# Kernel optimization log

Hardware: AMD Instinct MI355X
Metric: run time of the kernel (lower is better)

Reference implementation:

```python
import jax, jax.numpy as jnp
import numpy as np

B, N, M, C = 64, 16384, 64, 512
OUT = 3 * M + 6  # 198
EPS = 1e-8


def setup_inputs() -> dict:
    key = jax.random.key(0)
    k0, k1, k2, k3 = jax.random.split(key, 4)
    x = jax.random.normal(k0, (B, C), jnp.float32)
    # previous write weighting: a valid distribution over N rows
    w_prev = jax.nn.softmax(jax.random.normal(k1, (B, N), jnp.float32), axis=-1)
    memory = jax.random.normal(k2, (B, N, M), jnp.float32) * 0.1
    W = jax.random.normal(k3, (C, OUT), jnp.float32) * (1.0 / np.sqrt(C))
    b = jnp.zeros((OUT,), jnp.float32)
    return {"x": x, "w_prev": w_prev, "memory": memory, "W": W, "b": b}


def _address(memory, k, beta, g, s, gamma, w_prev):
    # content addressing: cosine similarity between key k [B,M] and memory [B,N,M]
    dot = jnp.einsum('bnm,bm->bn', memory, k)
    denom = jnp.linalg.norm(memory, axis=-1) * jnp.linalg.norm(k, axis=-1, keepdims=True) + EPS
    w_c = jax.nn.softmax(beta * dot / denom, axis=-1)          # [B,N]
    # interpolation gate
    w_g = g * w_c + (1.0 - g) * w_prev                          # [B,N]
    # circular convolution over shifts [-1, 0, +1]
    w_s = (s[:, 0:1] * jnp.roll(w_g, -1, axis=-1)
           + s[:, 1:2] * w_g
           + s[:, 2:3] * jnp.roll(w_g, 1, axis=-1))             # [B,N]
    # sharpening
    w_sharp = jnp.power(w_s + EPS, gamma)                       # gamma [B,1]
    return w_sharp / jnp.sum(w_sharp, axis=-1, keepdims=True)


def reference(x, w_prev, memory, W, b):
    proj = x @ W + b                                            # [B, 3M+6]
    k = proj[:, :M]
    beta = jax.nn.softplus(proj[:, M:M + 1])
    g = jax.nn.sigmoid(proj[:, M + 1:M + 2])
    s = jax.nn.softmax(proj[:, M + 2:M + 5], axis=-1)
    gamma = 1.0 + jax.nn.softplus(proj[:, M + 5:M + 6])
    e = jax.nn.sigmoid(proj[:, M + 6:M + 6 + M])
    a = proj[:, M + 6 + M:]
    w = _address(memory, k, beta, g, s, gamma, w_prev)          # [B,N]
    # erase-add write: mem' = mem * (1 - w^T e) + w^T a
    erase = jnp.einsum('bn,bm->bnm', w, e)
    add = jnp.einsum('bn,bm->bnm', w, a)
    mem_new = memory * (1.0 - erase) + add
    return proj, w, mem_new
```

## Files before the change

### kernel.cpp

```cpp
#include <hip/hip_runtime.h>
#include <math.h>

#define BB   64
#define NN   16384
#define MM   64
#define CIN  512
#define OUTD 198
#define EPSF 1e-8f

#define NCHUNK (NN / 256)
#define NBLK   (BB * NCHUNK)

__device__ inline float softplusf(float v) {
    return v > 20.f ? v : log1pf(expf(v));
}
__device__ inline float sigmoidf(float v) {
    return 1.f / (1.f + expf(-v));
}

__global__ __launch_bounds__(256) void proj_kernel(
    const float* __restrict__ x, const float* __restrict__ W,
    const float* __restrict__ bias, float* __restrict__ out_proj,
    float* __restrict__ scal)
{
    const int b = blockIdx.x;
    const int tid = threadIdx.x;
    __shared__ __align__(16) float xs[CIN];
    __shared__ float pr[OUTD];

    for (int c = tid; c < CIN; c += 256) xs[c] = x[b * CIN + c];
    __syncthreads();

    if (tid < OUTD) {
        float acc = bias[tid];
        #pragma unroll 8
        for (int c = 0; c < CIN; ++c)
            acc = fmaf(xs[c], W[c * OUTD + tid], acc);
        out_proj[b * OUTD + tid] = acc;
        pr[tid] = acc;
    }
    __syncthreads();

    if (tid == 0) {
        float beta  = softplusf(pr[MM]);
        float g     = sigmoidf(pr[MM + 1]);
        float s0r = pr[MM + 2], s1r = pr[MM + 3], s2r = pr[MM + 4];
        float mx  = fmaxf(s0r, fmaxf(s1r, s2r));
        float e0 = expf(s0r - mx), e1 = expf(s1r - mx), e2 = expf(s2r - mx);
        float inv = 1.f / (e0 + e1 + e2);
        float gamma = 1.f + softplusf(pr[MM + 5]);
        float ksq = 0.f;
        for (int m = 0; m < MM; ++m) ksq += pr[m] * pr[m];
        float* sc = scal + b * 8;
        sc[0] = beta; sc[1] = g;
        sc[2] = e0 * inv; sc[3] = e1 * inv; sc[4] = e2 * inv;
        sc[5] = gamma; sc[6] = sqrtf(ksq);
    }
}

__global__ __launch_bounds__(256) void score_kernel(
    const float* __restrict__ mem, const float* __restrict__ proj,
    const float* __restrict__ scal, float* __restrict__ score,
    float* __restrict__ partials)
{
    const int b     = blockIdx.x >> 6;
    const int chunk = blockIdx.x & 63;
    const int tid   = threadIdx.x;
    const int n     = chunk * 256 + tid;

    __shared__ __align__(16) float ks[MM];
    __shared__ float red[8];

    if (tid < MM) ks[tid] = proj[b * OUTD + tid];
    __syncthreads();

    const float4* row = (const float4*)(mem + ((size_t)b * NN + n) * MM);
    float dot = 0.f, nsq = 0.f;
    #pragma unroll
    for (int i = 0; i < MM / 4; ++i) {
        float4 v  = row[i];
        float4 kv = *(const float4*)(&ks[i * 4]);
        dot += v.x * kv.x + v.y * kv.y + v.z * kv.z + v.w * kv.w;
        nsq += v.x * v.x + v.y * v.y + v.z * v.z + v.w * v.w;
    }
    const float beta  = scal[b * 8 + 0];
    const float knorm = scal[b * 8 + 6];
    const float sc = beta * dot / (sqrtf(nsq) * knorm + EPSF);
    score[(size_t)b * NN + n] = sc;

    float mv = sc;
    #pragma unroll
    for (int o = 32; o > 0; o >>= 1) mv = fmaxf(mv, __shfl_xor(mv, o));
    const int wid = tid >> 6, lane = tid & 63;
    if (lane == 0) red[wid] = mv;
    __syncthreads();
    if (tid == 0) red[4] = fmaxf(fmaxf(red[0], red[1]), fmaxf(red[2], red[3]));
    __syncthreads();
    const float mb = red[4];

    float ex = expf(sc - mb);
    #pragma unroll
    for (int o = 32; o > 0; o >>= 1) ex += __shfl_xor(ex, o);
    if (lane == 0) red[wid] = ex;
    __syncthreads();
    if (tid == 0) {
        partials[2 * blockIdx.x]     = mb;
        partials[2 * blockIdx.x + 1] = red[0] + red[1] + red[2] + red[3];
    }
}

__global__ __launch_bounds__(64) void combine_kernel(
    const float* __restrict__ partials, float* __restrict__ Mb,
    float* __restrict__ Sb, float* __restrict__ sumW)
{
    const int b = blockIdx.x, t = threadIdx.x;
    const float mb = partials[2 * (b * NCHUNK + t)];
    const float sb = partials[2 * (b * NCHUNK + t) + 1];
    float M = mb;
    #pragma unroll
    for (int o = 32; o > 0; o >>= 1) M = fmaxf(M, __shfl_xor(M, o));
    float contrib = sb * expf(mb - M);
    #pragma unroll
    for (int o = 32; o > 0; o >>= 1) contrib += __shfl_xor(contrib, o);
    if (t == 0) { Mb[b] = M; Sb[b] = contrib; sumW[b] = 0.f; }
}

__global__ __launch_bounds__(256) void sharp_kernel(
    const float* __restrict__ score, const float* __restrict__ w_prev,
    const float* __restrict__ scal, const float* __restrict__ Mb,
    const float* __restrict__ Sb, float* __restrict__ wsharp,
    float* __restrict__ sumW)
{
    const int b     = blockIdx.x >> 6;
    const int chunk = blockIdx.x & 63;
    const int tid   = threadIdx.x;
    const int start = chunk * 256;

    __shared__ float wg[258];
    __shared__ float red[8];

    const float g    = scal[b * 8 + 1];
    const float Mv   = Mb[b];
    const float invS = 1.f / Sb[b];
    const float* scb = score  + (size_t)b * NN;
    const float* wpb = w_prev + (size_t)b * NN;

    for (int i = tid; i < 258; i += 256) {
        const int idx = (start - 1 + i + NN) & (NN - 1);
        const float wc = expf(scb[idx] - Mv) * invS;
        wg[i] = g * wc + (1.f - g) * wpb[idx];
    }
    __syncthreads();

    const float s0 = scal[b * 8 + 2], s1 = scal[b * 8 + 3];
    const float s2 = scal[b * 8 + 4], gamma = scal[b * 8 + 5];
    const float ws  = s0 * wg[tid + 2] + s1 * wg[tid + 1] + s2 * wg[tid];
    const float wsh = powf(ws + EPSF, gamma);
    wsharp[(size_t)b * NN + start + tid] = wsh;

    float sum = wsh;
    #pragma unroll
    for (int o = 32; o > 0; o >>= 1) sum += __shfl_xor(sum, o);
    const int wid = tid >> 6, lane = tid & 63;
    if (lane == 0) red[wid] = sum;
    __syncthreads();
    if (tid == 0) atomicAdd(&sumW[b], red[0] + red[1] + red[2] + red[3]);
}

__global__ __launch_bounds__(256) void update_kernel(
    const float* __restrict__ mem, const float* __restrict__ proj,
    const float* __restrict__ wsharp, const float* __restrict__ sumW,
    float* __restrict__ out_w, float* __restrict__ out_mem)
{
    const int blk   = (int)gridDim.x - 1 - (int)blockIdx.x;
    const int b     = blk >> 6;
    const int chunk = blk & 63;
    const int tid   = threadIdx.x;
    const int n     = chunk * 256 + tid;

    __shared__ __align__(16) float es[MM];
    __shared__ __align__(16) float as_[MM];
    if (tid < MM) {
        es[tid]  = sigmoidf(proj[b * OUTD + MM + 6 + tid]);
        as_[tid] = proj[b * OUTD + MM + 6 + MM + tid];
    }
    __syncthreads();

    const float w = wsharp[(size_t)b * NN + n] / sumW[b];
    out_w[(size_t)b * NN + n] = w;

    const float4* row  = (const float4*)(mem     + ((size_t)b * NN + n) * MM);
    float4*       orow = (float4*)      (out_mem + ((size_t)b * NN + n) * MM);
    #pragma unroll
    for (int i = 0; i < MM / 4; ++i) {
        const float4 v  = row[i];
        const float4 e4 = *(const float4*)(&es[i * 4]);
        const float4 a4 = *(const float4*)(&as_[i * 4]);
        float4 r;
        r.x = v.x * (1.f - w * e4.x) + w * a4.x;
        r.y = v.y * (1.f - w * e4.y) + w * a4.y;
        r.z = v.z * (1.f - w * e4.z) + w * a4.z;
        r.w = v.w * (1.f - w * e4.w) + w * a4.w;
        orow[i] = r;
    }
}

extern "C" void kernel_launch(void* const* d_in, const int* in_sizes, int n_in,
                              void* d_out, int out_size, void* d_ws, size_t ws_size,
                              hipStream_t stream)
{
    const float* x      = (const float*)d_in[0];
    const float* w_prev = (const float*)d_in[1];
    const float* memory = (const float*)d_in[2];
    const float* W      = (const float*)d_in[3];
    const float* bias   = (const float*)d_in[4];

    float* out      = (float*)d_out;
    float* out_proj = out;
    float* out_w    = out + BB * OUTD;
    float* out_mem  = out_w + (size_t)BB * NN;

    float* ws_f     = (float*)d_ws;
    float* score    = ws_f;
    float* wsharp   = score + (size_t)BB * NN;
    float* partials = wsharp + (size_t)BB * NN;
    float* Mb       = partials + 2 * NBLK;
    float* Sb       = Mb + BB;
    float* sumW     = Sb + BB;
    float* scal     = sumW + BB;

    proj_kernel   <<<BB,   256, 0, stream>>>(x, W, bias, out_proj, scal);
    score_kernel  <<<NBLK, 256, 0, stream>>>(memory, out_proj, scal, score, partials);
    combine_kernel<<<BB,    64, 0, stream>>>(partials, Mb, Sb, sumW);
    sharp_kernel  <<<NBLK, 256, 0, stream>>>(score, w_prev, scal, Mb, Sb, wsharp, sumW);
    update_kernel <<<NBLK, 256, 0, stream>>>(memory, out_proj, wsharp, sumW, out_w, out_mem);
}
```

Baseline: 657.4 us.

## Coalesce memory reads in score and update kernels via row-split thread mapping

The score kernel now has 16 threads cooperate on each 64-float row, reading contiguous float4s and reducing the dot product and norm with shuffles, in place of one thread striding across a whole row. The update kernel is remapped so each thread handles consecutive float4s of the flat memory array, with 16384 blocks each covering 4096 floats. The erase sigmoid and add vectors are precomputed once per batch row in proj_kernel. The aim is fully coalesced global loads and stores on the two passes that stream the 256MB memory tensor, at the cost of extra shuffle reductions and redundant w loads.

```diff
diff --git a/kernel.cpp b/kernel.cpp
--- a/kernel.cpp
+++ b/kernel.cpp
@@ -10,6 +10,7 @@
 
 #define NCHUNK (NN / 256)
 #define NBLK   (BB * NCHUNK)
+#define UPD_BLKS 16384
 
 __device__ inline float softplusf(float v) {
     return v > 20.f ? v : log1pf(expf(v));
@@ -21,7 +22,7 @@
 __global__ __launch_bounds__(256) void proj_kernel(
     const float* __restrict__ x, const float* __restrict__ W,
     const float* __restrict__ bias, float* __restrict__ out_proj,
-    float* __restrict__ scal)
+    float* __restrict__ scal, float* __restrict__ ea)
 {
     const int b = blockIdx.x;
     const int tid = threadIdx.x;
@@ -41,6 +42,10 @@
     }
     __syncthreads();
 
+    if (tid < MM) {
+        ea[b * 128 + tid]      = sigmoidf(pr[MM + 6 + tid]);
+        ea[b * 128 + 64 + tid] = pr[MM + 6 + MM + tid];
+    }
     if (tid == 0) {
         float beta  = softplusf(pr[MM]);
         float g     = sigmoidf(pr[MM + 1]);
@@ -66,28 +71,41 @@
     const int b     = blockIdx.x >> 6;
     const int chunk = blockIdx.x & 63;
     const int tid   = threadIdx.x;
-    const int n     = chunk * 256 + tid;
+    const int rowbase = chunk * 256;
 
     __shared__ __align__(16) float ks[MM];
+    __shared__ float rowsc[256];
     __shared__ float red[8];
 
     if (tid < MM) ks[tid] = proj[b * OUTD + tid];
     __syncthreads();
 
-    const float4* row = (const float4*)(mem + ((size_t)b * NN + n) * MM);
-    float dot = 0.f, nsq = 0.f;
-    #pragma unroll
-    for (int i = 0; i < MM / 4; ++i) {
-        float4 v  = row[i];
-        float4 kv = *(const float4*)(&ks[i * 4]);
-        dot += v.x * kv.x + v.y * kv.y + v.z * kv.z + v.w * kv.w;
-        nsq += v.x * v.x + v.y * v.y + v.z * v.z + v.w * v.w;
-    }
     const float beta  = scal[b * 8 + 0];
     const float knorm = scal[b * 8 + 6];
-    const float sc = beta * dot / (sqrtf(nsq) * knorm + EPSF);
-    score[(size_t)b * NN + n] = sc;
-
+    const int sub = tid & 15;
+    const int rg  = tid >> 4;
+    const float4 kv = *(const float4*)(&ks[sub * 4]);
+    const float4* base = (const float4*)(mem + ((size_t)b * NN + rowbase) * MM);
+
+    #pragma unroll
+    for (int it = 0; it < 16; ++it) {
+        const float4 v = base[(it * 16 + rg) * 16 + sub];
+        float dot = v.x * kv.x + v.y * kv.y + v.z * kv.z + v.w * kv.w;
+        float nsq = v.x * v.x + v.y * v.y + v.z * v.z + v.w * v.w;
+        #pragma unroll
+        for (int o = 1; o < 16; o <<= 1) {
+            dot += __shfl_xor(dot, o);
+            nsq += __shfl_xor(nsq, o);
+        }
+        if (sub == 0) {
+            const float sc = beta * dot / (sqrtf(nsq) * knorm + EPSF);
+            score[(size_t)b * NN + rowbase + it * 16 + rg] = sc;
+            rowsc[it * 16 + rg] = sc;
+        }
+    }
+    __syncthreads();
+
+    const float sc = rowsc[tid];
     float mv = sc;
     #pragma unroll
     for (int o = 32; o > 0; o >>= 1) mv = fmaxf(mv, __shfl_xor(mv, o));
@@ -168,40 +186,40 @@
 }
 
 __global__ __launch_bounds__(256) void update_kernel(
-    const float* __restrict__ mem, const float* __restrict__ proj,
+    const float* __restrict__ mem, const float* __restrict__ ea_g,
     const float* __restrict__ wsharp, const float* __restrict__ sumW,
     float* __restrict__ out_w, float* __restrict__ out_mem)
 {
-    const int blk   = (int)gridDim.x - 1 - (int)blockIdx.x;
-    const int b     = blk >> 6;
-    const int chunk = blk & 63;
-    const int tid   = threadIdx.x;
-    const int n     = chunk * 256 + tid;
-
-    __shared__ __align__(16) float es[MM];
-    __shared__ __align__(16) float as_[MM];
-    if (tid < MM) {
-        es[tid]  = sigmoidf(proj[b * OUTD + MM + 6 + tid]);
-        as_[tid] = proj[b * OUTD + MM + 6 + MM + tid];
-    }
-    __syncthreads();
-
-    const float w = wsharp[(size_t)b * NN + n] / sumW[b];
-    out_w[(size_t)b * NN + n] = w;
-
-    const float4* row  = (const float4*)(mem     + ((size_t)b * NN + n) * MM);
-    float4*       orow = (float4*)      (out_mem + ((size_t)b * NN + n) * MM);
-    #pragma unroll
-    for (int i = 0; i < MM / 4; ++i) {
-        const float4 v  = row[i];
-        const float4 e4 = *(const float4*)(&es[i * 4]);
-        const float4 a4 = *(const float4*)(&as_[i * 4]);
+    const int blk = UPD_BLKS - 1 - (int)blockIdx.x;
+    const int tid = threadIdx.x;
+    const int b   = blk >> 8;
+
+    __shared__ __align__(16) float ea[128];
+    if (tid < 32) *(float4*)(&ea[tid * 4]) =
+        *(const float4*)(&ea_g[b * 128 + tid * 4]);
+    __syncthreads();
+
+    const int m = (tid * 4) & 63;
+    const float4 e4 = *(const float4*)(&ea[m]);
+    const float4 a4 = *(const float4*)(&ea[64 + m]);
+    const float invS = 1.0f / sumW[b];
+    const size_t base_f = (size_t)blk * 4096;
+    const float* wsb = wsharp + (size_t)b * NN;
+    float*       owb = out_w  + (size_t)b * NN;
+
+    #pragma unroll
+    for (int it = 0; it < 4; ++it) {
+        const size_t off = base_f + (size_t)it * 1024 + tid * 4;
+        const int n = (int)((off >> 6) & (NN - 1));
+        const float w = wsb[n] * invS;
+        if ((tid & 15) == 0) owb[n] = w;
+        const float4 v = *(const float4*)(mem + off);
         float4 r;
         r.x = v.x * (1.f - w * e4.x) + w * a4.x;
         r.y = v.y * (1.f - w * e4.y) + w * a4.y;
         r.z = v.z * (1.f - w * e4.z) + w * a4.z;
         r.w = v.w * (1.f - w * e4.w) + w * a4.w;
-        orow[i] = r;
+        *(float4*)(out_mem + off) = r;
     }
 }
 
@@ -228,10 +246,11 @@
     float* Sb       = Mb + BB;
     float* sumW     = Sb + BB;
     float* scal     = sumW + BB;
-
-    proj_kernel   <<<BB,   256, 0, stream>>>(x, W, bias, out_proj, scal);
-    score_kernel  <<<NBLK, 256, 0, stream>>>(memory, out_proj, scal, score, partials);
-    combine_kernel<<<BB,    64, 0, stream>>>(partials, Mb, Sb, sumW);
-    sharp_kernel  <<<NBLK, 256, 0, stream>>>(score, w_prev, scal, Mb, Sb, wsharp, sumW);
-    update_kernel <<<NBLK, 256, 0, stream>>>(memory, out_proj, wsharp, sumW, out_w, out_mem);
-}
+    float* ea       = scal + 8 * BB;
+
+    proj_kernel   <<<BB,      256, 0, stream>>>(x, W, bias, out_proj, scal, ea);
+    score_kernel  <<<NBLK,    256, 0, stream>>>(memory, out_proj, scal, score, partials);
+    combine_kernel<<<BB,       64, 0, stream>>>(partials, Mb, Sb, sumW);
+    sharp_kernel  <<<NBLK,    256, 0, stream>>>(score, w_prev, scal, Mb, Sb, wsharp, sumW);
+    update_kernel <<<UPD_BLKS,256, 0, stream>>>(memory, ea, wsharp, sumW, out_w, out_mem);
+}
```

Measured after the change: 572.8 us. 12.9% less time.
